# Kernel tuning notes

Hardware: AMD Instinct MI355X
Metric: run time of the kernel (lower is better)

## Reference

```python
import jax, jax.numpy as jnp
import numpy as np

C = 512
HEADS = 4
GROUPS = 32
EPS = 1e-6


def setup_inputs() -> dict:
    key = jax.random.key(0)
    ks = jax.random.split(key, 6)
    s = 1.0 / np.sqrt(C)
    return {
        "x": jax.random.normal(ks[0], (2, C, 64, 64), dtype=jnp.float32),
        "gn_scale": jnp.ones((C,), jnp.float32),
        "gn_bias": jnp.zeros((C,), jnp.float32),
        "wq": jax.random.normal(ks[1], (C, C), jnp.float32) * s,
        "bq": jnp.zeros((C,), jnp.float32),
        "wk": jax.random.normal(ks[2], (C, C), jnp.float32) * s,
        "bk": jnp.zeros((C,), jnp.float32),
        "wv": jax.random.normal(ks[3], (C, C), jnp.float32) * s,
        "bv": jnp.zeros((C,), jnp.float32),
        "wo": jax.random.normal(ks[4], (C, C), jnp.float32) * s,
        "bo": jnp.zeros((C,), jnp.float32),
    }


def group_norm(x, scale, bias):
    # x: [b, c, h, w]; GroupNorm with 32 groups, eps 1e-6, affine
    b, c, h, w = x.shape
    xg = x.reshape(b, GROUPS, c // GROUPS, h, w)
    mean = jnp.mean(xg, axis=(2, 3, 4), keepdims=True)
    var = jnp.var(xg, axis=(2, 3, 4), keepdims=True)
    xg = (xg - mean) * jax.lax.rsqrt(var + EPS)
    x = xg.reshape(b, c, h, w)
    return x * scale[None, :, None, None] + bias[None, :, None, None]


def conv1x1(x, w, b):
    # 1x1 conv == per-pixel linear: [b,c,h,w] x [o,c] -> [b,o,h,w]
    return jnp.einsum('bchw,oc->bohw', x, w) + b[None, :, None, None]


def reference(x, gn_scale, gn_bias, wq, bq, wk, bk, wv, bv, wo, bo):
    b, c, h, w = x.shape
    hc = c // HEADS
    n = h * w

    h_ = group_norm(x, gn_scale, gn_bias)
    q = conv1x1(h_, wq, bq).reshape(b, HEADS, hc, n)
    k = conv1x1(h_, wk, bk).reshape(b, HEADS, hc, n)
    v = conv1x1(h_, wv, bv).reshape(b, HEADS, hc, n)

    # NOTE: scale uses full channel count c (repo quirk), not head_channel
    scale = jnp.asarray(c, x.dtype) ** -0.5
    scores = jnp.einsum('bhcn,bhcm->bhnm', q, k) * scale  # [b,H,N,N]
    attn = jax.nn.softmax(scores, axis=-1)
    out = jnp.einsum('bhnm,bhcm->bhcn', attn, v)  # [b,H,hc,N]

    out = out.reshape(b, c, h, w)
    return x + conv1x1(out, wo, bo)
```

## Files before the change

kernel.cpp:

```cpp
#include <hip/hip_runtime.h>

typedef float    f32x4 __attribute__((ext_vector_type(4)));
typedef short    bf16x8 __attribute__((ext_vector_type(8)));
typedef unsigned short u16;
typedef u16      u16x4 __attribute__((ext_vector_type(4)));
typedef unsigned u32;
typedef u32      u32x4 __attribute__((ext_vector_type(4)));

#define MFMA16(a, b, c) __builtin_amdgcn_mfma_f32_16x16x32_bf16((a), (b), (c), 0, 0, 0)

#define CCH 512
#define NPIX 4096
#define NHEAD 4
#define HC 128
#define NSPLIT 2
#define KVCHUNK (NPIX / NSPLIT)
#define QK_SCALE 0.04419417382415922f
#define LOG2E 1.4426950408889634f

__device__ __forceinline__ u16 f2b(float f) {
  unsigned u = __builtin_bit_cast(unsigned, f);
  u += 0x7FFFu + ((u >> 16) & 1u);
  return (u16)(u >> 16);
}
__device__ __forceinline__ float b2f(u16 b) {
  return __builtin_bit_cast(float, ((unsigned)b) << 16);
}

__device__ __forceinline__ void gl_lds16(const u16* g, u16* l) {
  __builtin_amdgcn_global_load_lds((const __attribute__((address_space(1))) void*)g,
                                   (__attribute__((address_space(3))) void*)l, 16, 0, 0);
}

__global__ void prep_k(const float* __restrict__ w0, const float* __restrict__ w1,
                       const float* __restrict__ w2, const float* __restrict__ w3,
                       u16* __restrict__ dst,
                       const float* __restrict__ x, float* __restrict__ pstats) {
  int blk = blockIdx.x, t = threadIdx.x;
  if (blk < 1024) {
    int m = blk >> 8;
    const float* src = (m == 0) ? w0 : (m == 1) ? w1 : (m == 2) ? w2 : w3;
    int i = ((blk & 255) * 256 + t) * 4;
    f32x4 v = *(const f32x4*)(src + i);
    u16x4 o = { f2b(v[0]), f2b(v[1]), f2b(v[2]), f2b(v[3]) };
    *(u16x4*)(dst + (size_t)m * (CCH * CCH) + i) = o;
    return;
  }
  int sblk = blk - 1024;
  const f32x4* p = (const f32x4*)(x + (size_t)sblk * 16384);
  int wv = t >> 6, l = t & 63;
  float s = 0.f, ss = 0.f;
  for (int i = t; i < 4096; i += 256) {
    f32x4 v = p[i];
    s  += v[0] + v[1] + v[2] + v[3];
    ss += v[0]*v[0] + v[1]*v[1] + v[2]*v[2] + v[3]*v[3];
  }
  #pragma unroll
  for (int d = 32; d; d >>= 1) { s += __shfl_down(s, d, 64); ss += __shfl_down(ss, d, 64); }
  __shared__ float red[8];
  if (l == 0) { red[wv*2] = s; red[wv*2+1] = ss; }
  __syncthreads();
  if (t == 0) {
    pstats[sblk*2]   = red[0] + red[2] + red[4] + red[6];
    pstats[sblk*2+1] = red[1] + red[3] + red[5] + red[7];
  }
}

__global__ void gn_norm_k(const float* __restrict__ x, const float* __restrict__ gns,
                          const float* __restrict__ gnb, const float* __restrict__ pstats,
                          u16* __restrict__ Ht) {
  int t = threadIdx.x;
  int ct = blockIdx.x * 64, nt = blockIdx.y * 64, b = blockIdx.z;
  int c0 = ct + (t & 15) * 4;
  int n0 = nt + (t >> 4) * 4;
  const float* xb = x + ((size_t)b * CCH + c0) * NPIX + n0;
  int g = b * 32 + (c0 >> 4);
  const f32x4* ps = (const f32x4*)(pstats + g * 8);
  f32x4 p0 = ps[0], p1 = ps[1];
  float s  = p0[0] + p0[2] + p1[0] + p1[2];
  float ss = p0[1] + p0[3] + p1[1] + p1[3];
  float mean = s * (1.f/65536.f);
  float var  = ss * (1.f/65536.f) - mean*mean;
  float rstd = rsqrtf(var + 1e-6f);
  f32x4 rows[4];
  #pragma unroll
  for (int j = 0; j < 4; ++j) {
    f32x4 v = *(const f32x4*)(xb + (size_t)j * NPIX);
    float a  = rstd * gns[c0 + j];
    float bb = gnb[c0 + j] - mean * a;
    rows[j] = v * a + bb;
  }
  #pragma unroll
  for (int i = 0; i < 4; ++i) {
    u16x4 o = { f2b(rows[0][i]), f2b(rows[1][i]), f2b(rows[2][i]), f2b(rows[3][i]) };
    *(u16x4*)(Ht + ((size_t)b * NPIX + n0 + i) * CCH + c0) = o;
  }
}

template<int MODE>
__global__ __launch_bounds__(256) void gemm_nt(const u16* __restrict__ A,
                                               const u16* __restrict__ B,
                                               const float* __restrict__ bias,
                                               const float* __restrict__ bias2,
                                               u16* __restrict__ outb,
                                               u16* __restrict__ outb2,
                                               float* __restrict__ outf,
                                               const float* __restrict__ resid,
                                               float alpha) {
  __shared__ __align__(16) u16 As[2][128 * 32];
  __shared__ __align__(16) u16 Bs[2][128 * 32];
  const int t = threadIdx.x, l = t & 63, wv = t >> 6;
  const int l16 = l & 15, lq = l >> 4;
  const int mt = blockIdx.x * 128, nt = blockIdx.y * 128, z = blockIdx.z;
  const u16* Ap = A + (size_t)mt * CCH;
  const u16* Bp = (MODE == 3) ? (B + (size_t)nt * CCH)
                              : (B + ((size_t)z * NPIX + nt) * CCH);
  const int wm = (wv >> 1) * 64, wn = (wv & 1) * 64;
  f32x4 acc[4][4] = {};

  #pragma unroll
  for (int j = 0; j < 2; ++j) {
    int idx = t + j * 256;
    int row = idx >> 2, kc = (idx & 3) * 8;
    gl_lds16(Ap + (size_t)row * CCH + kc, &As[0][0] + idx * 8);
    gl_lds16(Bp + (size_t)row * CCH + kc, &Bs[0][0] + idx * 8);
  }
  asm volatile("s_waitcnt vmcnt(0)" ::: "memory");
  __syncthreads();

#define GEMM_BODY(CUR, K0, DOSTAGE)                                                   \
  {                                                                                   \
    if (DOSTAGE) {                                                                    \
      _Pragma("unroll")                                                               \
      for (int j = 0; j < 2; ++j) {                                                   \
        int idx = t + j * 256;                                                        \
        int row = idx >> 2, kc = (idx & 3) * 8;                                       \
        gl_lds16(Ap + (size_t)row * CCH + (K0) + 32 + kc, &As[(CUR) ^ 1][0] + idx * 8); \
        gl_lds16(Bp + (size_t)row * CCH + (K0) + 32 + kc, &Bs[(CUR) ^ 1][0] + idx * 8); \
      }                                                                               \
    }                                                                                 \
    bf16x8 af[4], bfr[4];                                                             \
    _Pragma("unroll")                                                                 \
    for (int i = 0; i < 4; ++i) {                                                     \
      af[i]  = *(const bf16x8*)(&As[CUR][0] + (wm + i * 16 + l16) * 32 + lq * 8);     \
      bfr[i] = *(const bf16x8*)(&Bs[CUR][0] + (wn + i * 16 + l16) * 32 + lq * 8);     \
    }                                                                                 \
    _Pragma("unroll")                                                                 \
    for (int mi = 0; mi < 4; ++mi)                                                    \
      _Pragma("unroll")                                                               \
      for (int ni = 0; ni < 4; ++ni)                                                  \
        acc[mi][ni] = MFMA16(af[mi], bfr[ni], acc[mi][ni]);                           \
    asm volatile("s_waitcnt vmcnt(0)" ::: "memory");                                  \
    __syncthreads();                                                                  \
  }

  for (int k0 = 0; k0 < CCH; k0 += 64) {
    GEMM_BODY(0, k0, true)
    GEMM_BODY(1, k0 + 32, (k0 + 64 < CCH))
  }
#undef GEMM_BODY

  #pragma unroll
  for (int mi = 0; mi < 4; ++mi)
    #pragma unroll
    for (int ni = 0; ni < 4; ++ni)
      #pragma unroll
      for (int r = 0; r < 4; ++r) {
        int grow = mt + wm + mi * 16 + lq * 4 + r;
        int gcol = nt + wn + ni * 16 + l16;
        float v = acc[mi][ni][r];
        if (MODE == 1) {
          outb[((size_t)z * CCH + grow) * NPIX + gcol] = f2b(v + bias[grow]);
        } else if (MODE == 2) {
          size_t off = ((size_t)z * CCH + grow) * NPIX + gcol;
          outf[off] = v + bias[grow] + resid[off];
        } else {
          if (gcol < 512)
            outb[(size_t)grow * CCH + gcol] = f2b((v + bias[gcol]) * alpha);
          else
            outb2[(size_t)grow * CCH + (gcol - 512)] = f2b(v + bias2[gcol - 512]);
        }
      }
}

__global__ __launch_bounds__(256, 2) void flash_k(const u16* __restrict__ Qt,
                                                  const u16* __restrict__ Kt,
                                                  const u16* __restrict__ Vc,
                                                  u16* __restrict__ sl0, u16* __restrict__ sl1,
                                                  float* __restrict__ mlp) {
  __shared__ __align__(16) char lds[65536];
  const int t = threadIdx.x, wv = t >> 6, l = t & 63;
  const int l16 = l & 15, lq = l >> 4;
  const int orig = blockIdx.x;
  const int gid = (orig & 7) * 64 + (orig >> 3);
  const int qx = gid & 31, grp = gid >> 5;
  const int hd = grp & 3, b = (grp >> 2) & 1, s = grp >> 3;
  const int qt0 = qx * 128 + wv * 32;

  const u16* Q = Qt + ((size_t)b * NPIX + qt0) * CCH + hd * HC;
  const u16* Kbase = Kt + (size_t)b * NPIX * CCH + hd * HC;
  const u16* Vbase = Vc + (size_t)b * CCH * NPIX + (size_t)hd * HC * NPIX;
  u16* slab = (s == 0) ? sl0 : sl1;
  u16* Ob = slab + ((size_t)(b * NHEAD + hd) * NPIX + qt0) * HC;
  size_t mlR0 = (size_t)s * 32768 + (size_t)(b * NHEAD + hd) * NPIX + qt0;

  bf16x8 qf[2][4];
  #pragma unroll
  for (int mi = 0; mi < 2; ++mi)
    #pragma unroll
    for (int kk = 0; kk < 4; ++kk)
      qf[mi][kk] = *(const bf16x8*)(Q + (size_t)(mi * 16 + l16) * CCH + kk * 32 + lq * 8);

  const int m_beg = s * KVCHUNK;
  const int sw = (l16 & 7) << 4;
  const int vb2 = (lq & 1) * 32 + (lq >> 1) * 16;

  int kbase[4], vbase[2];
  #pragma unroll
  for (int kk = 0; kk < 4; ++kk) kbase[kk] = l16 * 256 + ((kk * 64 + lq * 16) ^ sw);
  #pragma unroll
  for (int ks = 0; ks < 2; ++ks) vbase[ks] = 32768 + l16 * 128 + ((ks * 64 + vb2) ^ sw);

  u32 kgo[4], vgo[4];
  #pragma unroll
  for (int j = 0; j < 4; ++j) {
    int g = j * 256 + t;
    { int row = g >> 4, src = ((g & 15) << 4) ^ ((row & 7) << 4);
      kgo[j] = (u32)row * CCH + (src >> 1); }
    { int row = g >> 3, src = ((g & 7) << 4) ^ ((row & 7) << 4);
      vgo[j] = (u32)row * NPIX + (src >> 1); }
  }

  const short one_bf = (short)0x3F80;
  const bf16x8 vones = { one_bf, one_bf, one_bf, one_bf, one_bf, one_bf, one_bf, one_bf };

  f32x4 oacc[2][8] = {};
  f32x4 osum[2] = {};

  {
    const u16* kg = Kbase + (size_t)m_beg * CCH;
    const u16* vg = Vbase + m_beg;
    #pragma unroll
    for (int j = 0; j < 4; ++j) {
      gl_lds16(kg + kgo[j], (u16*)lds + (j * 256 + t) * 8);
      gl_lds16(vg + vgo[j], (u16*)(lds + 32768) + (j * 256 + t) * 8);
    }
  }
  asm volatile("s_waitcnt vmcnt(0)" ::: "memory");
  __syncthreads();

  const int NT = KVCHUNK / 64;

#define FLASH_BODY(CUR, M0, DOSTAGE)                                                   \
  {                                                                                    \
    if (DOSTAGE) {                                                                     \
      const u16* kg = Kbase + (size_t)((M0) + 64) * CCH;                               \
      const u16* vg = Vbase + ((M0) + 64);                                             \
      _Pragma("unroll")                                                                \
      for (int j = 0; j < 4; ++j) {                                                    \
        gl_lds16(kg + kgo[j], (u16*)(lds + ((CUR) ^ 1) * 16384) + (j * 256 + t) * 8);  \
        gl_lds16(vg + vgo[j], (u16*)(lds + 32768 + ((CUR) ^ 1) * 16384) + (j * 256 + t) * 8); \
      }                                                                                \
    }                                                                                  \
    f32x4 S[2][4] = {};                                                                \
    __builtin_amdgcn_s_setprio(1);                                                     \
    _Pragma("unroll")                                                                  \
    for (int kk = 0; kk < 4; ++kk)                                                     \
      _Pragma("unroll")                                                                \
      for (int mm = 0; mm < 4; ++mm) {                                                 \
        bf16x8 kf = *(const bf16x8*)(lds + kbase[kk] + mm * 4096 + (CUR) * 16384);     \
        S[0][mm] = MFMA16(kf, qf[0][kk], S[0][mm]);                                    \
        S[1][mm] = MFMA16(kf, qf[1][kk], S[1][mm]);                                    \
      }                                                                                \
    __builtin_amdgcn_s_setprio(0);                                                     \
    u32 pk[2][4][2];                                                                   \
    _Pragma("unroll")                                                                  \
    for (int mi = 0; mi < 2; ++mi) {                                                   \
      _Pragma("unroll")                                                                \
      for (int mm = 0; mm < 4; ++mm) {                                                 \
        f32x4 p;                                                                       \
        _Pragma("unroll")                                                              \
        for (int r = 0; r < 4; ++r) p[r] = exp2f(S[mi][mm][r]);                        \
        asm("v_cvt_pk_bf16_f32 %0, %1, %2" : "=v"(pk[mi][mm][0]) : "v"(p[0]), "v"(p[1])); \
        asm("v_cvt_pk_bf16_f32 %0, %1, %2" : "=v"(pk[mi][mm][1]) : "v"(p[2]), "v"(p[3])); \
      }                                                                                \
    }                                                                                  \
    bf16x8 pa[2][2];                                                                   \
    _Pragma("unroll")                                                                  \
    for (int mi = 0; mi < 2; ++mi)                                                     \
      _Pragma("unroll")                                                                \
      for (int ks = 0; ks < 2; ++ks) {                                                 \
        u32 a0 = pk[mi][2 * ks][0], a1 = pk[mi][2 * ks][1];                            \
        u32 b0 = pk[mi][2 * ks + 1][0], b1 = pk[mi][2 * ks + 1][1];                    \
        asm("v_permlane16_swap_b32 %0, %1" : "+v"(a0), "+v"(b0));                      \
        asm("v_permlane16_swap_b32 %0, %1" : "+v"(a1), "+v"(b1));                      \
        u32x4 w = { a0, a1, b0, b1 };                                                  \
        pa[mi][ks] = __builtin_bit_cast(bf16x8, w);                                    \
      }                                                                                \
    __builtin_amdgcn_s_setprio(1);                                                     \
    _Pragma("unroll")                                                                  \
    for (int ks = 0; ks < 2; ++ks) {                                                   \
      osum[0] = MFMA16(pa[0][ks], vones, osum[0]);                                     \
      osum[1] = MFMA16(pa[1][ks], vones, osum[1]);                                     \
      _Pragma("unroll")                                                                \
      for (int cc = 0; cc < 8; ++cc) {                                                 \
        bf16x8 vf = *(const bf16x8*)(lds + vbase[ks] + cc * 2048 + (CUR) * 16384);     \
        oacc[0][cc] = MFMA16(pa[0][ks], vf, oacc[0][cc]);                              \
        oacc[1][cc] = MFMA16(pa[1][ks], vf, oacc[1][cc]);                              \
      }                                                                                \
    }                                                                                  \
    __builtin_amdgcn_s_setprio(0);                                                     \
    asm volatile("s_waitcnt vmcnt(0)" ::: "memory");                                   \
    __syncthreads();                                                                   \
  }

  for (int it = 0; it < NT; it += 2) {
    FLASH_BODY(0, m_beg + it * 64, true)
    FLASH_BODY(1, m_beg + it * 64 + 64, (it + 2 < NT))
  }
#undef FLASH_BODY

  #pragma unroll
  for (int mi = 0; mi < 2; ++mi)
    #pragma unroll
    for (int cc = 0; cc < 8; ++cc)
      #pragma unroll
      for (int r = 0; r < 4; ++r)
        Ob[(size_t)(mi * 16 + lq * 4 + r) * HC + cc * 16 + l16] = f2b(oacc[mi][cc][r]);
  if (l16 == 0) {
    #pragma unroll
    for (int mi = 0; mi < 2; ++mi)
      #pragma unroll
      for (int r = 0; r < 4; ++r)
        mlp[mlR0 + mi * 16 + lq * 4 + r] = osum[mi][r];
  }
}

__global__ void merge_k(const u16* __restrict__ s0, const u16* __restrict__ s1,
                        const float* __restrict__ ml, u16* __restrict__ Ot) {
  int t = threadIdx.x;
  int R = blockIdx.x * 32 + (t >> 3);
  int ch = (t & 7) * 16;
  float L = ml[R] + ml[32768 + R];
  float inv = 1.f / L;
  float acc[16] = {};
  const u16* sp[2] = { s0, s1 };
  #pragma unroll
  for (int s = 0; s < 2; ++s) {
    const bf16x8* p = (const bf16x8*)(sp[s] + (size_t)R * HC + ch);
    #pragma unroll
    for (int j = 0; j < 2; ++j) {
      bf16x8 v = p[j];
      #pragma unroll
      for (int e = 0; e < 8; ++e) acc[j * 8 + e] += b2f((u16)v[e]);
    }
  }
  int b = R >> 14, h = (R >> 12) & 3, q = R & 4095;
  u16* o = Ot + ((size_t)((b << 12) + q) * CCH) + h * HC + ch;
  #pragma unroll
  for (int j = 0; j < 4; ++j) {
    u16x4 o4 = { f2b(acc[j*4] * inv), f2b(acc[j*4+1] * inv),
                 f2b(acc[j*4+2] * inv), f2b(acc[j*4+3] * inv) };
    *(u16x4*)(o + j * 4) = o4;
  }
}

extern "C" void kernel_launch(void* const* d_in, const int* in_sizes, int n_in,
                              void* d_out, int out_size, void* d_ws, size_t ws_size,
                              hipStream_t stream) {
  const float* x   = (const float*)d_in[0];
  const float* gns = (const float*)d_in[1];
  const float* gnb = (const float*)d_in[2];
  const float* wq  = (const float*)d_in[3];
  const float* bq  = (const float*)d_in[4];
  const float* wk  = (const float*)d_in[5];
  const float* bk  = (const float*)d_in[6];
  const float* wv  = (const float*)d_in[7];
  const float* bv  = (const float*)d_in[8];
  const float* wo  = (const float*)d_in[9];
  const float* bo  = (const float*)d_in[10];
  float* out = (float*)d_out;
  char* ws = (char*)d_ws;

  u16*   wb    = (u16*)ws;
  u16*   Ht    = (u16*)(ws + (size_t)( 2u << 20));
  u16*   Qt    = (u16*)(ws + (size_t)(10u << 20));
  u16*   Kt    = (u16*)(ws + (size_t)(18u << 20));
  u16*   Vc    = (u16*)(ws + (size_t)(26u << 20));
  u16*   Ot    = (u16*)(ws + (size_t)(34u << 20));
  float* mlb   = (float*)(ws + (size_t)(42u << 20));
  float* stats = (float*)(ws + (size_t)(43u << 20));
  u16*   sl0   = Ht;
  u16*   sl1   = (u16*)d_out;

  prep_k    <<<dim3(1280, 1, 1), 256, 0, stream>>>(wq, wk, wv, wo, wb, x, stats);
  gn_norm_k <<<dim3(8, 64, 2),  256, 0, stream>>>(x, gns, gnb, stats, Ht);
  gemm_nt<3><<<dim3(64, 8, 1),  256, 0, stream>>>(Ht, wb, bq, bk, Qt, Kt, nullptr, nullptr,
                                                  QK_SCALE * LOG2E);
  gemm_nt<1><<<dim3(4, 32, 2),  256, 0, stream>>>(wb + 2u * 262144u, Ht, bv, nullptr, Vc, nullptr,
                                                  nullptr, nullptr, 1.0f);
  flash_k   <<<dim3(512, 1, 1), 256, 0, stream>>>(Qt, Kt, Vc, sl0, sl1, mlb);
  merge_k   <<<dim3(1024, 1, 1),256, 0, stream>>>(sl0, sl1, mlb, Ot);
  gemm_nt<2><<<dim3(4, 32, 2),  256, 0, stream>>>(wb + 3u * 262144u, Ot, bo, nullptr, nullptr,
                                                  nullptr, out, x, 1.0f);
}
```

Measured before the change: 153.5 us.

## Fuse split-KV merge into output projection GEMM and merge QKV launches

Folds the split-KV merge into the output projection GEMM. That GEMM now reads both partial attention outputs, accumulates the two MFMA products, and rescales the accumulators per head using the stored softmax sums. This removes the merge kernel and the round trip through the Ot buffer. The Q/K and V projection GEMMs are also combined into one launch that dispatches on block index. The cost is more LDS per block, twice the B-operand loads and MFMAs in the output GEMM, and a rescaling step between heads whose ratio of partial sums could lose precision.

After: 147.5 us. 1.04x faster.

```diff
diff --git a/kernel.cpp b/kernel.cpp
--- a/kernel.cpp
+++ b/kernel.cpp
@@ -98,20 +98,18 @@
 }
 
 template<int MODE>
-__global__ __launch_bounds__(256) void gemm_nt(const u16* __restrict__ A,
-                                               const u16* __restrict__ B,
-                                               const float* __restrict__ bias,
-                                               const float* __restrict__ bias2,
-                                               u16* __restrict__ outb,
-                                               u16* __restrict__ outb2,
-                                               float* __restrict__ outf,
-                                               const float* __restrict__ resid,
-                                               float alpha) {
-  __shared__ __align__(16) u16 As[2][128 * 32];
-  __shared__ __align__(16) u16 Bs[2][128 * 32];
+__device__ __forceinline__ void gemm_body(const u16* __restrict__ A,
+                                          const u16* __restrict__ B,
+                                          const float* __restrict__ bias,
+                                          const float* __restrict__ bias2,
+                                          u16* __restrict__ outb,
+                                          u16* __restrict__ outb2,
+                                          float alpha,
+                                          int bx, int by, int z,
+                                          u16* As, u16* Bs) {
   const int t = threadIdx.x, l = t & 63, wv = t >> 6;
   const int l16 = l & 15, lq = l >> 4;
-  const int mt = blockIdx.x * 128, nt = blockIdx.y * 128, z = blockIdx.z;
+  const int mt = bx * 128, nt = by * 128;
   const u16* Ap = A + (size_t)mt * CCH;
   const u16* Bp = (MODE == 3) ? (B + (size_t)nt * CCH)
                               : (B + ((size_t)z * NPIX + nt) * CCH);
@@ -122,8 +120,8 @@
   for (int j = 0; j < 2; ++j) {
     int idx = t + j * 256;
     int row = idx >> 2, kc = (idx & 3) * 8;
-    gl_lds16(Ap + (size_t)row * CCH + kc, &As[0][0] + idx * 8);
-    gl_lds16(Bp + (size_t)row * CCH + kc, &Bs[0][0] + idx * 8);
+    gl_lds16(Ap + (size_t)row * CCH + kc, As + idx * 8);
+    gl_lds16(Bp + (size_t)row * CCH + kc, Bs + idx * 8);
   }
   asm volatile("s_waitcnt vmcnt(0)" ::: "memory");
   __syncthreads();
@@ -135,15 +133,15 @@
       for (int j = 0; j < 2; ++j) {                                                   \
         int idx = t + j * 256;                                                        \
         int row = idx >> 2, kc = (idx & 3) * 8;                                       \
-        gl_lds16(Ap + (size_t)row * CCH + (K0) + 32 + kc, &As[(CUR) ^ 1][0] + idx * 8); \
-        gl_lds16(Bp + (size_t)row * CCH + (K0) + 32 + kc, &Bs[(CUR) ^ 1][0] + idx * 8); \
+        gl_lds16(Ap + (size_t)row * CCH + (K0) + 32 + kc, As + ((CUR) ^ 1) * 4096 + idx * 8); \
+        gl_lds16(Bp + (size_t)row * CCH + (K0) + 32 + kc, Bs + ((CUR) ^ 1) * 4096 + idx * 8); \
       }                                                                               \
     }                                                                                 \
     bf16x8 af[4], bfr[4];                                                             \
     _Pragma("unroll")                                                                 \
     for (int i = 0; i < 4; ++i) {                                                     \
-      af[i]  = *(const bf16x8*)(&As[CUR][0] + (wm + i * 16 + l16) * 32 + lq * 8);     \
-      bfr[i] = *(const bf16x8*)(&Bs[CUR][0] + (wn + i * 16 + l16) * 32 + lq * 8);     \
+      af[i]  = *(const bf16x8*)(As + (CUR) * 4096 + (wm + i * 16 + l16) * 32 + lq * 8); \
+      bfr[i] = *(const bf16x8*)(Bs + (CUR) * 4096 + (wn + i * 16 + l16) * 32 + lq * 8); \
     }                                                                                 \
     _Pragma("unroll")                                                                 \
     for (int mi = 0; mi < 4; ++mi)                                                    \
@@ -171,9 +169,6 @@
         float v = acc[mi][ni][r];
         if (MODE == 1) {
           outb[((size_t)z * CCH + grow) * NPIX + gcol] = f2b(v + bias[grow]);
-        } else if (MODE == 2) {
-          size_t off = ((size_t)z * CCH + grow) * NPIX + gcol;
-          outf[off] = v + bias[grow] + resid[off];
         } else {
           if (gcol < 512)
             outb[(size_t)grow * CCH + gcol] = f2b((v + bias[gcol]) * alpha);
@@ -181,6 +176,26 @@
             outb2[(size_t)grow * CCH + (gcol - 512)] = f2b(v + bias2[gcol - 512]);
         }
       }
+}
+
+__global__ __launch_bounds__(256) void qkv_k(const u16* __restrict__ Ht,
+                                             const u16* __restrict__ wb,
+                                             const float* __restrict__ bq,
+                                             const float* __restrict__ bk,
+                                             const float* __restrict__ bv,
+                                             u16* __restrict__ Qt, u16* __restrict__ Kt,
+                                             u16* __restrict__ Vc, float alpha) {
+  __shared__ __align__(16) u16 As[2][4096];
+  __shared__ __align__(16) u16 Bs[2][4096];
+  int blk = blockIdx.x;
+  if (blk < 512) {
+    gemm_body<3>(Ht, wb, bq, bk, Qt, Kt, alpha, blk & 63, blk >> 6, 0,
+                 &As[0][0], &Bs[0][0]);
+  } else {
+    int r = blk - 512;
+    gemm_body<1>(wb + 2u * 262144u, Ht, bv, nullptr, Vc, nullptr, 1.0f,
+                 r & 3, (r >> 2) & 31, r >> 7, &As[0][0], &Bs[0][0]);
+  }
 }
 
 __global__ __launch_bounds__(256, 2) void flash_k(const u16* __restrict__ Qt,
@@ -336,32 +351,108 @@
   }
 }
 
-__global__ void merge_k(const u16* __restrict__ s0, const u16* __restrict__ s1,
-                        const float* __restrict__ ml, u16* __restrict__ Ot) {
-  int t = threadIdx.x;
-  int R = blockIdx.x * 32 + (t >> 3);
-  int ch = (t & 7) * 16;
-  float L = ml[R] + ml[32768 + R];
-  float inv = 1.f / L;
-  float acc[16] = {};
-  const u16* sp[2] = { s0, s1 };
-  #pragma unroll
-  for (int s = 0; s < 2; ++s) {
-    const bf16x8* p = (const bf16x8*)(sp[s] + (size_t)R * HC + ch);
-    #pragma unroll
-    for (int j = 0; j < 2; ++j) {
-      bf16x8 v = p[j];
+__global__ __launch_bounds__(256) void fgemm_k(const u16* __restrict__ Wo,
+                                               const u16* __restrict__ sl0,
+                                               const u16* __restrict__ sl1,
+                                               const float* __restrict__ ml,
+                                               const float* __restrict__ bias,
+                                               const float* __restrict__ resid,
+                                               float* __restrict__ outf) {
+  __shared__ __align__(16) u16 As[2][4096];
+  __shared__ __align__(16) u16 B0[2][4096];
+  __shared__ __align__(16) u16 B1[2][4096];
+  const int t = threadIdx.x, l = t & 63, wv = t >> 6;
+  const int l16 = l & 15, lq = l >> 4;
+  const int mt = blockIdx.x * 128, nt = blockIdx.y * 128, z = blockIdx.z;
+  const u16* Ap = Wo + (size_t)mt * CCH;
+  const int wm = (wv >> 1) * 64, wn = (wv & 1) * 64;
+
+  float lsum[4][4];
+  #pragma unroll
+  for (int h = 0; h < 4; ++h)
+    #pragma unroll
+    for (int ni = 0; ni < 4; ++ni) {
+      int gcol = nt + wn + ni * 16 + l16;
+      int R = ((z * 4 + h) << 12) + gcol;
+      lsum[h][ni] = ml[R] + ml[32768 + R];
+    }
+
+  f32x4 acc[4][4] = {};
+
+  #pragma unroll
+  for (int j = 0; j < 2; ++j) {
+    int idx = t + j * 256;
+    int row = idx >> 2, kc = (idx & 3) * 8;
+    gl_lds16(Ap + (size_t)row * CCH + kc, &As[0][0] + idx * 8);
+    size_t srow = ((size_t)(z * 4) * NPIX + nt + row) * HC + kc;
+    gl_lds16(sl0 + srow, &B0[0][0] + idx * 8);
+    gl_lds16(sl1 + srow, &B1[0][0] + idx * 8);
+  }
+  asm volatile("s_waitcnt vmcnt(0)" ::: "memory");
+  __syncthreads();
+
+#define FG_BODY(CUR, K0, DOSTAGE)                                                     \
+  {                                                                                   \
+    if (DOSTAGE) {                                                                    \
+      const int kn = (K0) + 32;                                                       \
+      const int hn = kn >> 7, cn = kn & 127;                                          \
+      _Pragma("unroll")                                                               \
+      for (int j = 0; j < 2; ++j) {                                                   \
+        int idx = t + j * 256;                                                        \
+        int row = idx >> 2, kc = (idx & 3) * 8;                                       \
+        gl_lds16(Ap + (size_t)row * CCH + kn + kc, &As[(CUR) ^ 1][0] + idx * 8);      \
+        size_t srow = ((size_t)(z * 4 + hn) * NPIX + nt + row) * HC + cn + kc;        \
+        gl_lds16(sl0 + srow, &B0[(CUR) ^ 1][0] + idx * 8);                            \
+        gl_lds16(sl1 + srow, &B1[(CUR) ^ 1][0] + idx * 8);                            \
+      }                                                                               \
+    }                                                                                 \
+    bf16x8 af[4], b0f[4], b1f[4];                                                     \
+    _Pragma("unroll")                                                                 \
+    for (int i = 0; i < 4; ++i) {                                                     \
+      af[i]  = *(const bf16x8*)(&As[CUR][0] + (wm + i * 16 + l16) * 32 + lq * 8);     \
+      b0f[i] = *(const bf16x8*)(&B0[CUR][0] + (wn + i * 16 + l16) * 32 + lq * 8);     \
+      b1f[i] = *(const bf16x8*)(&B1[CUR][0] + (wn + i * 16 + l16) * 32 + lq * 8);     \
+    }                                                                                 \
+    _Pragma("unroll")                                                                 \
+    for (int mi = 0; mi < 4; ++mi)                                                    \
+      _Pragma("unroll")                                                               \
+      for (int ni = 0; ni < 4; ++ni) {                                                \
+        acc[mi][ni] = MFMA16(af[mi], b0f[ni], acc[mi][ni]);                           \
+        acc[mi][ni] = MFMA16(af[mi], b1f[ni], acc[mi][ni]);                           \
+      }                                                                               \
+    asm volatile("s_waitcnt vmcnt(0)" ::: "memory");                                  \
+    __syncthreads();                                                                  \
+  }
+
+  #pragma unroll
+  for (int h = 0; h < 4; ++h) {
+    if (h) {
       #pragma unroll
-      for (int e = 0; e < 8; ++e) acc[j * 8 + e] += b2f((u16)v[e]);
+      for (int ni = 0; ni < 4; ++ni) {
+        float rat = lsum[h][ni] / lsum[h - 1][ni];
+        #pragma unroll
+        for (int mi = 0; mi < 4; ++mi) acc[mi][ni] *= rat;
+      }
     }
-  }
-  int b = R >> 14, h = (R >> 12) & 3, q = R & 4095;
-  u16* o = Ot + ((size_t)((b << 12) + q) * CCH) + h * HC + ch;
-  #pragma unroll
-  for (int j = 0; j < 4; ++j) {
-    u16x4 o4 = { f2b(acc[j*4] * inv), f2b(acc[j*4+1] * inv),
-                 f2b(acc[j*4+2] * inv), f2b(acc[j*4+3] * inv) };
-    *(u16x4*)(o + j * 4) = o4;
+    FG_BODY(0, h * 128,      true)
+    FG_BODY(1, h * 128 + 32, true)
+    FG_BODY(0, h * 128 + 64, true)
+    FG_BODY(1, h * 128 + 96, (h < 3))
+  }
+#undef FG_BODY
+
+  #pragma unroll
+  for (int ni = 0; ni < 4; ++ni) {
+    float inv3 = 1.f / lsum[3][ni];
+    int gcol = nt + wn + ni * 16 + l16;
+    #pragma unroll
+    for (int mi = 0; mi < 4; ++mi)
+      #pragma unroll
+      for (int r = 0; r < 4; ++r) {
+        int grow = mt + wm + mi * 16 + lq * 4 + r;
+        size_t off = ((size_t)z * CCH + grow) * NPIX + gcol;
+        outf[off] = acc[mi][ni][r] * inv3 + bias[grow] + resid[off];
+      }
   }
 }
 
@@ -387,20 +478,16 @@
   u16*   Qt    = (u16*)(ws + (size_t)(10u << 20));
   u16*   Kt    = (u16*)(ws + (size_t)(18u << 20));
   u16*   Vc    = (u16*)(ws + (size_t)(26u << 20));
-  u16*   Ot    = (u16*)(ws + (size_t)(34u << 20));
+  u16*   sl1   = (u16*)(ws + (size_t)(34u << 20));
   float* mlb   = (float*)(ws + (size_t)(42u << 20));
   float* stats = (float*)(ws + (size_t)(43u << 20));
   u16*   sl0   = Ht;
-  u16*   sl1   = (u16*)d_out;
 
   prep_k    <<<dim3(1280, 1, 1), 256, 0, stream>>>(wq, wk, wv, wo, wb, x, stats);
-  gn_norm_k <<<dim3(8, 64, 2),  256, 0, stream>>>(x, gns, gnb, stats, Ht);
-  gemm_nt<3><<<dim3(64, 8, 1),  256, 0, stream>>>(Ht, wb, bq, bk, Qt, Kt, nullptr, nullptr,
-                                                  QK_SCALE * LOG2E);
-  gemm_nt<1><<<dim3(4, 32, 2),  256, 0, stream>>>(wb + 2u * 262144u, Ht, bv, nullptr, Vc, nullptr,
-                                                  nullptr, nullptr, 1.0f);
-  flash_k   <<<dim3(512, 1, 1), 256, 0, stream>>>(Qt, Kt, Vc, sl0, sl1, mlb);
-  merge_k   <<<dim3(1024, 1, 1),256, 0, stream>>>(sl0, sl1, mlb, Ot);
-  gemm_nt<2><<<dim3(4, 32, 2),  256, 0, stream>>>(wb + 3u * 262144u, Ot, bo, nullptr, nullptr,
-                                                  nullptr, out, x, 1.0f);
-}
+  gn_norm_k <<<dim3(8, 64, 2),   256, 0, stream>>>(x, gns, gnb, stats, Ht);
+  qkv_k     <<<dim3(768, 1, 1),  256, 0, stream>>>(Ht, wb, bq, bk, bv, Qt, Kt, Vc,
+                                                   QK_SCALE * LOG2E);
+  flash_k   <<<dim3(512, 1, 1),  256, 0, stream>>>(Qt, Kt, Vc, sl0, sl1, mlb);
+  fgemm_k   <<<dim3(4, 32, 2),   256, 0, stream>>>(wb + 3u * 262144u, sl0, sl1, mlb,
+                                                   bo, x, out);
+}
```
